# Kernel tuning notes

Measured on AMD Instinct MI355X. Metric: run time of the kernel, lower is better.

## Reference

```python
import jax, jax.numpy as jnp
import numpy as np

B, T, K = 512, 1024, 48          # batch, seq_len, n_tokens
START, END = 46, 47              # token_dict['START'], token_dict['END']
NEG = -10000.0


def setup_inputs() -> dict:
    key = jax.random.key(0)
    k1, k2 = jax.random.split(key)
    feats = jax.random.normal(k1, (B, T, K), dtype=jnp.float32)
    transitions = jax.random.normal(k2, (K, K), dtype=jnp.float32)
    return {"feats": feats, "transitions": transitions}


def _mask_transitions(transitions):
    # Mirrors __init__: no transition out of END-column target / into START row.
    t = transitions.at[START, :].set(NEG)
    t = t.at[:, END].set(NEG)
    return t


def _crf_logz(feats, trans):
    """forward_prop: CRF forward algorithm. feats [T,K], trans [K_next,K_prev]."""
    init = jnp.full((K,), NEG, feats.dtype).at[START].set(0.0)

    def step(alpha, feat):
        # scores[next, prev] = alpha[prev] + trans[next, prev] + feat[next]
        scores = alpha[None, :] + trans + feat[:, None]
        return jax.nn.logsumexp(scores, axis=1), None

    alpha, _ = jax.lax.scan(step, init, feats)
    return jax.nn.logsumexp(alpha + trans[END])


def _viterbi(feats, trans):
    """viterbi_decode: max-product recurrence + backtrace. feats [T,K]."""
    init = jnp.full((K,), NEG, feats.dtype).at[START].set(0.0)

    def step(v, feat):
        # NOTE: original takes argmax BEFORE adding emission, then adds feat.
        scores = v[None, :] + trans          # [K_next, K_prev]
        bp = jnp.argmax(scores, axis=1)      # backpointers [K]
        return jnp.max(scores, axis=1) + feat, bp

    v, bptrs = jax.lax.scan(step, init, feats)   # bptrs [T, K]
    term = v + trans[END]
    last = jnp.argmax(term)
    path_score = term[last]

    def back(tag, bp):
        return bp[tag], tag

    _, path = jax.lax.scan(back, last, bptrs, reverse=True)  # path [T]
    return path_score, path


def reference(feats, transitions):
    trans = _mask_transitions(transitions)
    logz = jax.vmap(lambda f: _crf_logz(f, trans))(feats)          # [B]
    scores, paths = jax.vmap(lambda f: _viterbi(f, trans))(feats)  # [B], [B,T]
    return logz, scores, paths
```

## Files before the change

### kernel.cpp

```cpp
#include <hip/hip_runtime.h>

#define NB 512
#define NT 1024
#define NK 48
#define NEGV -10000.0f
#define S_START 46
#define S_END 47

__device__ __forceinline__ float rfl_f32(float x) {
    return __int_as_float(__builtin_amdgcn_readfirstlane(__float_as_int(x)));
}

extern "C" __global__ __launch_bounds__(128, 1)
void crf_fused(const float* __restrict__ feats, const float* __restrict__ trans,
               float* __restrict__ out)
{
    __shared__ unsigned char bp[NT * NK];
    __shared__ unsigned char comp[64 * NK];
    __shared__ unsigned char boundary[64];
    __shared__ float eabuf[64];
    __shared__ float vbuf[64];

    const int b = blockIdx.x;
    const int wave = threadIdx.x >> 6;
    const int lane = threadIdx.x & 63;
    const bool act = lane < NK;
    const int LL = act ? lane : (NK - 1);
    const float* f = feats + (size_t)b * NT * NK;
    const float* fb = f + LL;

    float tEnd = NEGV;
    if (act && lane != S_END) tEnd = trans[S_END * NK + lane];

    if (wave == 0) {
        float Erow[NK];
        {
            const bool rowdead = (lane == S_START);
            const float4* r4 = (const float4*)(trans + LL * NK);
            #pragma unroll
            for (int q = 0; q < NK / 4; ++q) {
                float4 r = r4[q];
                const int c = 4 * q;
                Erow[c + 0] = (rowdead || c + 0 == S_END) ? 0.0f : __expf(r.x);
                Erow[c + 1] = (rowdead || c + 1 == S_END) ? 0.0f : __expf(r.y);
                Erow[c + 2] = (rowdead || c + 2 == S_END) ? 0.0f : __expf(r.z);
                Erow[c + 3] = (rowdead || c + 3 == S_END) ? 0.0f : __expf(r.w);
            }
        }
        float u = (lane == S_START) ? 0.0f : NEGV;
        float Muni = 0.0f;
        eabuf[lane] = __expf(u);
        __builtin_amdgcn_wave_barrier();

        float fr0 = fb[0 * NK], fr1 = fb[1 * NK], fr2 = fb[2 * NK], fr3 = fb[3 * NK];

        auto fstep = [&](float fc) {
            float ea[NK];
            {
                const float4* e4 = (const float4*)eabuf;
                #pragma unroll
                for (int q = 0; q < NK / 4; ++q) {
                    float4 r = e4[q];
                    ea[4 * q + 0] = r.x; ea[4 * q + 1] = r.y;
                    ea[4 * q + 2] = r.z; ea[4 * q + 3] = r.w;
                }
            }
            float a0 = 0.f, a1 = 0.f, a2 = 0.f, a3 = 0.f;
            #pragma unroll
            for (int p = 0; p < NK; p += 4) {
                a0 = fmaf(Erow[p + 0], ea[p + 0], a0);
                a1 = fmaf(Erow[p + 1], ea[p + 1], a1);
                a2 = fmaf(Erow[p + 2], ea[p + 2], a2);
                a3 = fmaf(Erow[p + 3], ea[p + 3], a3);
            }
            float acc = (a0 + a1) + (a2 + a3);
            float w = __logf(acc) + fc;
            float dM = rfl_f32(w);
            Muni += dM;
            u = w - dM;
            __builtin_amdgcn_wave_barrier();
            eabuf[lane] = __expf(u);
            __builtin_amdgcn_wave_barrier();
        };

        for (int t = 0; t < NT; t += 4) {
            { float fc = fr0; int nr = (t + 4 < NT) ? t + 4 : NT - 1; fr0 = fb[nr * NK]; fstep(fc); }
            { float fc = fr1; int nr = (t + 5 < NT) ? t + 5 : NT - 1; fr1 = fb[nr * NK]; fstep(fc); }
            { float fc = fr2; int nr = (t + 6 < NT) ? t + 6 : NT - 1; fr2 = fb[nr * NK]; fstep(fc); }
            { float fc = fr3; int nr = (t + 7 < NT) ? t + 7 : NT - 1; fr3 = fb[nr * NK]; fstep(fc); }
        }
        float x = act ? (u + tEnd) : -INFINITY;
        float M2 = x;
        #pragma unroll
        for (int off = 32; off >= 1; off >>= 1)
            M2 = fmaxf(M2, __shfl_xor(M2, off, 64));
        float e = __expf(x - M2);
        #pragma unroll
        for (int off = 32; off >= 1; off >>= 1)
            e += __shfl_xor(e, off, 64);
        if (lane == 0) out[b] = Muni + M2 + __logf(e);
    } else {
        float trow[NK];
        {
            const bool rowdead = (lane == S_START);
            const float4* r4 = (const float4*)(trans + LL * NK);
            #pragma unroll
            for (int q = 0; q < NK / 4; ++q) {
                float4 r = r4[q];
                const int c = 4 * q;
                trow[c + 0] = (rowdead || c + 0 == S_END) ? NEGV : r.x;
                trow[c + 1] = (rowdead || c + 1 == S_END) ? NEGV : r.y;
                trow[c + 2] = (rowdead || c + 2 == S_END) ? NEGV : r.z;
                trow[c + 3] = (rowdead || c + 3 == S_END) ? NEGV : r.w;
            }
        }
        float v = (lane == S_START) ? 0.0f : NEGV;
        vbuf[lane] = v;
        __builtin_amdgcn_wave_barrier();

        float fr0 = fb[0 * NK], fr1 = fb[1 * NK], fr2 = fb[2 * NK], fr3 = fb[3 * NK];
        const int big = 63;

        auto vstep = [&](float fc, int tt) {
            float s[NK];
            {
                const float4* v4 = (const float4*)vbuf;
                #pragma unroll
                for (int q = 0; q < NK / 4; ++q) {
                    float4 r = v4[q];
                    s[4 * q + 0] = r.x + trow[4 * q + 0];
                    s[4 * q + 1] = r.y + trow[4 * q + 1];
                    s[4 * q + 2] = r.z + trow[4 * q + 2];
                    s[4 * q + 3] = r.w + trow[4 * q + 3];
                }
            }
            float m16[16];
            #pragma unroll
            for (int i = 0; i < 16; ++i)
                m16[i] = fmaxf(fmaxf(s[3 * i], s[3 * i + 1]), s[3 * i + 2]);
            float m6[6];
            #pragma unroll
            for (int i = 0; i < 5; ++i)
                m6[i] = fmaxf(fmaxf(m16[3 * i], m16[3 * i + 1]), m16[3 * i + 2]);
            m6[5] = m16[15];
            float best = fmaxf(fmaxf(fmaxf(m6[0], m6[1]), m6[2]),
                               fmaxf(fmaxf(m6[3], m6[4]), m6[5]));
            v = best + fc;
            __builtin_amdgcn_wave_barrier();
            vbuf[lane] = v;
            __builtin_amdgcn_wave_barrier();
            int ix[NK];
            #pragma unroll
            for (int p = 0; p < NK; ++p)
                ix[p] = (s[p] != best) ? big : p;
            int n16[16];
            #pragma unroll
            for (int i = 0; i < 16; ++i)
                n16[i] = min(min(ix[3 * i], ix[3 * i + 1]), ix[3 * i + 2]);
            int n6[6];
            #pragma unroll
            for (int i = 0; i < 5; ++i)
                n6[i] = min(min(n16[3 * i], n16[3 * i + 1]), n16[3 * i + 2]);
            n6[5] = n16[15];
            int bi = min(min(min(n6[0], n6[1]), n6[2]),
                         min(min(n6[3], n6[4]), n6[5]));

            bp[tt * NK + LL] = (unsigned char)bi;
        };

        for (int t = 0; t < NT; t += 4) {
            { float fc = fr0; int nr = (t + 4 < NT) ? t + 4 : NT - 1; fr0 = fb[nr * NK]; vstep(fc, t + 0); }
            { float fc = fr1; int nr = (t + 5 < NT) ? t + 5 : NT - 1; fr1 = fb[nr * NK]; vstep(fc, t + 1); }
            { float fc = fr2; int nr = (t + 6 < NT) ? t + 6 : NT - 1; fr2 = fb[nr * NK]; vstep(fc, t + 2); }
            { float fc = fr3; int nr = (t + 7 < NT) ? t + 7 : NT - 1; fr3 = fb[nr * NK]; vstep(fc, t + 3); }
        }
        float xv = act ? (v + tEnd) : -INFINITY;
        int idx = act ? lane : 63;
        float val = xv;
        #pragma unroll
        for (int off = 32; off >= 1; off >>= 1) {
            float ov = __shfl_xor(val, off, 64);
            int   oi = __shfl_xor(idx, off, 64);
            if (ov > val || (ov == val && oi < idx)) { val = ov; idx = oi; }
        }
        if (lane == 0) out[NB + b] = val;
        const int last = idx;

        __builtin_amdgcn_wave_barrier();
        int cur[NK];
        #pragma unroll
        for (int k = 0; k < NK; ++k) cur[k] = k;
        const int tbase = lane * 16;
        for (int i = 15; i >= 0; --i) {
            const int t = tbase + i;
            #pragma unroll
            for (int k = 0; k < NK; ++k) cur[k] = bp[t * NK + cur[k]];
        }
        #pragma unroll
        for (int k = 0; k < NK; ++k) comp[lane * NK + k] = (unsigned char)cur[k];
        __builtin_amdgcn_wave_barrier();

        if (lane == 0) {
            int tag = last;
            for (int l = 63; l >= 0; --l) {
                boundary[l] = (unsigned char)tag;
                tag = comp[l * NK + tag];
            }
        }
        __builtin_amdgcn_wave_barrier();

        int tag = boundary[lane];
        float* pout = out + 2 * NB + (size_t)b * NT;
        for (int i = 15; i >= 0; --i) {
            const int t = tbase + i;
            pout[t] = (float)tag;
            tag = bp[t * NK + tag];
        }
    }
}

extern "C" void kernel_launch(void* const* d_in, const int* in_sizes, int n_in,
                              void* d_out, int out_size, void* d_ws, size_t ws_size,
                              hipStream_t stream) {
    (void)in_sizes; (void)n_in; (void)d_ws; (void)ws_size; (void)out_size;
    const float* feats = (const float*)d_in[0];
    const float* trans = (const float*)d_in[1];
    float* out = (float*)d_out;
    crf_fused<<<dim3(NB), dim3(128), 0, stream>>>(feats, trans, out);
}
```

Baseline: 528.4 us.

## Offload Viterbi argmax and chunk composition to helper waves via checkpoint replay

Grows the block from two waves to four. The main Viterbi wave now runs only the max recurrence and saves its state at each 16-step chunk boundary. Two helper waves take turns replaying each chunk from that checkpoint; they compute the argmax backpointers and build the per-chunk composed backpointer map with ds_bpermute. This takes the argmax and index-composition work off the serial critical path. In exchange the max work is done twice and a block-wide __syncthreads is added every 16 steps, which also stalls the forward (logZ) wave.

New measurement: 495.6 us. 6.2% less time.

```diff
diff --git a/kernel.cpp b/kernel.cpp
--- a/kernel.cpp
+++ b/kernel.cpp
@@ -6,20 +6,24 @@
 #define NEGV -10000.0f
 #define S_START 46
 #define S_END 47
+#define NCH 64
+#define CLEN 16
 
 __device__ __forceinline__ float rfl_f32(float x) {
     return __int_as_float(__builtin_amdgcn_readfirstlane(__float_as_int(x)));
 }
 
-extern "C" __global__ __launch_bounds__(128, 1)
+extern "C" __global__ __launch_bounds__(256, 1)
 void crf_fused(const float* __restrict__ feats, const float* __restrict__ trans,
                float* __restrict__ out)
 {
     __shared__ unsigned char bp[NT * NK];
-    __shared__ unsigned char comp[64 * NK];
-    __shared__ unsigned char boundary[64];
+    __shared__ float ckpt[4 * NK];
+    __shared__ unsigned char comp[NCH * NK];
+    __shared__ unsigned char boundary[NCH];
     __shared__ float eabuf[64];
-    __shared__ float vbuf[64];
+    __shared__ float vbuf1[64];
+    __shared__ float vbufw[2][64];
 
     const int b = blockIdx.x;
     const int wave = threadIdx.x >> 6;
@@ -51,7 +55,6 @@
         float Muni = 0.0f;
         eabuf[lane] = __expf(u);
         __builtin_amdgcn_wave_barrier();
-
         float fr0 = fb[0 * NK], fr1 = fb[1 * NK], fr2 = fb[2 * NK], fr3 = fb[3 * NK];
 
         auto fstep = [&](float fc) {
@@ -83,11 +86,19 @@
             __builtin_amdgcn_wave_barrier();
         };
 
-        for (int t = 0; t < NT; t += 4) {
-            { float fc = fr0; int nr = (t + 4 < NT) ? t + 4 : NT - 1; fr0 = fb[nr * NK]; fstep(fc); }
-            { float fc = fr1; int nr = (t + 5 < NT) ? t + 5 : NT - 1; fr1 = fb[nr * NK]; fstep(fc); }
-            { float fc = fr2; int nr = (t + 6 < NT) ? t + 6 : NT - 1; fr2 = fb[nr * NK]; fstep(fc); }
-            { float fc = fr3; int nr = (t + 7 < NT) ? t + 7 : NT - 1; fr3 = fb[nr * NK]; fstep(fc); }
+        __syncthreads();
+        for (int it = 0; it <= NCH; ++it) {
+            if (it < NCH) {
+                #pragma unroll
+                for (int g = 0; g < 4; ++g) {
+                    const int t = it * CLEN + 4 * g;
+                    { float fc = fr0; int nr = (t + 4 < NT) ? t + 4 : NT - 1; fr0 = fb[nr * NK]; fstep(fc); }
+                    { float fc = fr1; int nr = (t + 5 < NT) ? t + 5 : NT - 1; fr1 = fb[nr * NK]; fstep(fc); }
+                    { float fc = fr2; int nr = (t + 6 < NT) ? t + 6 : NT - 1; fr2 = fb[nr * NK]; fstep(fc); }
+                    { float fc = fr3; int nr = (t + 7 < NT) ? t + 7 : NT - 1; fr3 = fb[nr * NK]; fstep(fc); }
+                }
+            }
+            __syncthreads();
         }
         float x = act ? (u + tEnd) : -INFINITY;
         float M2 = x;
@@ -99,7 +110,7 @@
         for (int off = 32; off >= 1; off >>= 1)
             e += __shfl_xor(e, off, 64);
         if (lane == 0) out[b] = Muni + M2 + __logf(e);
-    } else {
+    } else if (wave == 1) {
         float trow[NK];
         {
             const bool rowdead = (lane == S_START);
@@ -115,16 +126,15 @@
             }
         }
         float v = (lane == S_START) ? 0.0f : NEGV;
-        vbuf[lane] = v;
+        vbuf1[lane] = v;
+        if (act) ckpt[0 * NK + lane] = v;
         __builtin_amdgcn_wave_barrier();
-
         float fr0 = fb[0 * NK], fr1 = fb[1 * NK], fr2 = fb[2 * NK], fr3 = fb[3 * NK];
-        const int big = 63;
-
-        auto vstep = [&](float fc, int tt) {
+
+        auto vstep = [&](float fc) {
             float s[NK];
             {
-                const float4* v4 = (const float4*)vbuf;
+                const float4* v4 = (const float4*)vbuf1;
                 #pragma unroll
                 for (int q = 0; q < NK / 4; ++q) {
                     float4 r = v4[q];
@@ -147,74 +157,148 @@
                                fmaxf(fmaxf(m6[3], m6[4]), m6[5]));
             v = best + fc;
             __builtin_amdgcn_wave_barrier();
-            vbuf[lane] = v;
+            vbuf1[lane] = v;
             __builtin_amdgcn_wave_barrier();
-            int ix[NK];
-            #pragma unroll
-            for (int p = 0; p < NK; ++p)
-                ix[p] = (s[p] != best) ? big : p;
-            int n16[16];
-            #pragma unroll
-            for (int i = 0; i < 16; ++i)
-                n16[i] = min(min(ix[3 * i], ix[3 * i + 1]), ix[3 * i + 2]);
-            int n6[6];
-            #pragma unroll
-            for (int i = 0; i < 5; ++i)
-                n6[i] = min(min(n16[3 * i], n16[3 * i + 1]), n16[3 * i + 2]);
-            n6[5] = n16[15];
-            int bi = min(min(min(n6[0], n6[1]), n6[2]),
-                         min(min(n6[3], n6[4]), n6[5]));
-
-            bp[tt * NK + LL] = (unsigned char)bi;
         };
 
-        for (int t = 0; t < NT; t += 4) {
-            { float fc = fr0; int nr = (t + 4 < NT) ? t + 4 : NT - 1; fr0 = fb[nr * NK]; vstep(fc, t + 0); }
-            { float fc = fr1; int nr = (t + 5 < NT) ? t + 5 : NT - 1; fr1 = fb[nr * NK]; vstep(fc, t + 1); }
-            { float fc = fr2; int nr = (t + 6 < NT) ? t + 6 : NT - 1; fr2 = fb[nr * NK]; vstep(fc, t + 2); }
-            { float fc = fr3; int nr = (t + 7 < NT) ? t + 7 : NT - 1; fr3 = fb[nr * NK]; vstep(fc, t + 3); }
-        }
-        float xv = act ? (v + tEnd) : -INFINITY;
-        int idx = act ? lane : 63;
-        float val = xv;
-        #pragma unroll
-        for (int off = 32; off >= 1; off >>= 1) {
-            float ov = __shfl_xor(val, off, 64);
-            int   oi = __shfl_xor(idx, off, 64);
-            if (ov > val || (ov == val && oi < idx)) { val = ov; idx = oi; }
-        }
-        if (lane == 0) out[NB + b] = val;
-        const int last = idx;
-
-        __builtin_amdgcn_wave_barrier();
-        int cur[NK];
-        #pragma unroll
-        for (int k = 0; k < NK; ++k) cur[k] = k;
-        const int tbase = lane * 16;
-        for (int i = 15; i >= 0; --i) {
-            const int t = tbase + i;
-            #pragma unroll
-            for (int k = 0; k < NK; ++k) cur[k] = bp[t * NK + cur[k]];
-        }
-        #pragma unroll
-        for (int k = 0; k < NK; ++k) comp[lane * NK + k] = (unsigned char)cur[k];
-        __builtin_amdgcn_wave_barrier();
-
+        int last = 0;
+        __syncthreads();
+        for (int it = 0; it <= NCH; ++it) {
+            if (it < NCH) {
+                #pragma unroll
+                for (int g = 0; g < 4; ++g) {
+                    const int t = it * CLEN + 4 * g;
+                    { float fc = fr0; int nr = (t + 4 < NT) ? t + 4 : NT - 1; fr0 = fb[nr * NK]; vstep(fc); }
+                    { float fc = fr1; int nr = (t + 5 < NT) ? t + 5 : NT - 1; fr1 = fb[nr * NK]; vstep(fc); }
+                    { float fc = fr2; int nr = (t + 6 < NT) ? t + 6 : NT - 1; fr2 = fb[nr * NK]; vstep(fc); }
+                    { float fc = fr3; int nr = (t + 7 < NT) ? t + 7 : NT - 1; fr3 = fb[nr * NK]; vstep(fc); }
+                }
+                if (act && it + 1 < NCH) ckpt[((it + 1) & 3) * NK + lane] = v;
+            } else {
+                float xv = act ? (v + tEnd) : -INFINITY;
+                int idx = act ? lane : 63;
+                float val = xv;
+                #pragma unroll
+                for (int off = 32; off >= 1; off >>= 1) {
+                    float ov = __shfl_xor(val, off, 64);
+                    int   oi = __shfl_xor(idx, off, 64);
+                    if (ov > val || (ov == val && oi < idx)) { val = ov; idx = oi; }
+                }
+                if (lane == 0) out[NB + b] = val;
+                last = idx;
+            }
+            __syncthreads();
+        }
         if (lane == 0) {
             int tag = last;
-            for (int l = 63; l >= 0; --l) {
+            for (int l = NCH - 1; l >= 0; --l) {
                 boundary[l] = (unsigned char)tag;
                 tag = comp[l * NK + tag];
             }
         }
         __builtin_amdgcn_wave_barrier();
-
         int tag = boundary[lane];
         float* pout = out + 2 * NB + (size_t)b * NT;
-        for (int i = 15; i >= 0; --i) {
-            const int t = tbase + i;
-            pout[t] = (float)tag;
-            tag = bp[t * NK + tag];
+        const int tbase = lane * CLEN;
+        for (int i = CLEN - 1; i >= 0; --i) {
+            pout[tbase + i] = (float)tag;
+            tag = bp[(tbase + i) * NK + tag];
+        }
+    } else {
+        const int w = wave - 2;
+        float trow[NK];
+        {
+            const bool rowdead = (lane == S_START);
+            const float4* r4 = (const float4*)(trans + LL * NK);
+            #pragma unroll
+            for (int q = 0; q < NK / 4; ++q) {
+                float4 r = r4[q];
+                const int c = 4 * q;
+                trow[c + 0] = (rowdead || c + 0 == S_END) ? NEGV : r.x;
+                trow[c + 1] = (rowdead || c + 1 == S_END) ? NEGV : r.y;
+                trow[c + 2] = (rowdead || c + 2 == S_END) ? NEGV : r.z;
+                trow[c + 3] = (rowdead || c + 3 == S_END) ? NEGV : r.w;
+            }
+        }
+        float* vbw = vbufw[w];
+        const int big = 63;
+        int bpl[8], bph[8];
+
+        auto replay8 = [&](int c, int base, int* bparr8) {
+            const float* fbc = fb + (size_t)c * CLEN * NK;
+            unsigned char* bpc = bp + (size_t)c * CLEN * NK;
+            float fv[8];
+            #pragma unroll
+            for (int i = 0; i < 8; ++i) fv[i] = fbc[(base + i) * NK];
+            #pragma unroll
+            for (int i = 0; i < 8; ++i) {
+                float s[NK];
+                {
+                    const float4* v4 = (const float4*)vbw;
+                    #pragma unroll
+                    for (int q = 0; q < NK / 4; ++q) {
+                        float4 r = v4[q];
+                        s[4 * q + 0] = r.x + trow[4 * q + 0];
+                        s[4 * q + 1] = r.y + trow[4 * q + 1];
+                        s[4 * q + 2] = r.z + trow[4 * q + 2];
+                        s[4 * q + 3] = r.w + trow[4 * q + 3];
+                    }
+                }
+                float m16[16];
+                #pragma unroll
+                for (int j = 0; j < 16; ++j)
+                    m16[j] = fmaxf(fmaxf(s[3 * j], s[3 * j + 1]), s[3 * j + 2]);
+                float m6[6];
+                #pragma unroll
+                for (int j = 0; j < 5; ++j)
+                    m6[j] = fmaxf(fmaxf(m16[3 * j], m16[3 * j + 1]), m16[3 * j + 2]);
+                m6[5] = m16[15];
+                float best = fmaxf(fmaxf(fmaxf(m6[0], m6[1]), m6[2]),
+                                   fmaxf(fmaxf(m6[3], m6[4]), m6[5]));
+                int ix[NK];
+                #pragma unroll
+                for (int p = 0; p < NK; ++p)
+                    ix[p] = (s[p] != best) ? big : p;
+                int n16[16];
+                #pragma unroll
+                for (int j = 0; j < 16; ++j)
+                    n16[j] = min(min(ix[3 * j], ix[3 * j + 1]), ix[3 * j + 2]);
+                int n6[6];
+                #pragma unroll
+                for (int j = 0; j < 5; ++j)
+                    n6[j] = min(min(n16[3 * j], n16[3 * j + 1]), n16[3 * j + 2]);
+                n6[5] = n16[15];
+                int bi = min(min(min(n6[0], n6[1]), n6[2]),
+                             min(min(n6[3], n6[4]), n6[5]));
+
+                bparr8[i] = bi;
+                bpc[(base + i) * NK + LL] = (unsigned char)bi;
+                float vn = best + fv[i];
+                __builtin_amdgcn_wave_barrier();
+                vbw[lane] = vn;
+                __builtin_amdgcn_wave_barrier();
+            }
+        };
+
+        __syncthreads();
+        for (int it = 0; it <= NCH; ++it) {
+            if ((it & 1) == w && it < NCH) {
+                vbw[lane] = ckpt[(it & 3) * NK + LL];
+                __builtin_amdgcn_wave_barrier();
+                replay8(it, 0, bpl);
+            } else if ((it & 1) != w && it >= 1) {
+                const int c = it - 1;
+                replay8(c, 8, bph);
+                int tag = act ? lane : 0;
+                #pragma unroll
+                for (int i = 7; i >= 0; --i)
+                    tag = __builtin_amdgcn_ds_bpermute(tag << 2, bph[i]);
+                #pragma unroll
+                for (int i = 7; i >= 0; --i)
+                    tag = __builtin_amdgcn_ds_bpermute(tag << 2, bpl[i]);
+                if (act) comp[c * NK + lane] = (unsigned char)tag;
+            }
+            __syncthreads();
         }
     }
 }
@@ -226,5 +310,5 @@
     const float* feats = (const float*)d_in[0];
     const float* trans = (const float*)d_in[1];
     float* out = (float*)d_out;
-    crf_fused<<<dim3(NB), dim3(128), 0, stream>>>(feats, trans, out);
+    crf_fused<<<dim3(NB), dim3(256), 0, stream>>>(feats, trans, out);
 }
```
